# Optimization experiments

Measured on AMD Instinct MI355X. Metric: run time of the kernel, lower is better.

## Reference

```python
import jax, jax.numpy as jnp
import numpy as np

B, S, D, H = 8, 1024, 1024, 16
DH = D // H  # 64

def setup_inputs() -> dict:
    key = jax.random.key(0)
    k1, k2, k3 = jax.random.split(key, 3)
    x = jax.random.normal(k1, (B, S, D), dtype=jnp.float32)
    mask = jnp.tril(jnp.ones((S, S), dtype=bool))[None, None]  # causal [1,1,S,S]
    W_qkv = jax.random.normal(k2, (D, 3 * D), dtype=jnp.float32) * 0.02
    W_out = jax.random.normal(k3, (D, D), dtype=jnp.float32) * 0.02
    return {"x": x, "mask": mask, "W_qkv": W_qkv, "W_out": W_out}

def reference(x, mask, W_qkv, W_out):
    qkv = jnp.einsum('bnd,de->bne', x, W_qkv)
    q, k, v = jnp.split(qkv, 3, axis=-1)
    # [b, h, n, dh]
    split_heads = lambda t: t.reshape(B, S, H, DH).transpose(0, 2, 1, 3)
    q, k, v = map(split_heads, (q, k, v))
    attn = jnp.einsum('bhnd,bhmd->bhnm', q, k) / jnp.sqrt(jnp.float32(DH))
    attn = jnp.where(mask, attn, 0.7 * jnp.finfo(attn.dtype).min)
    attn = jax.nn.softmax(attn.astype(jnp.float32), axis=-1).astype(x.dtype)
    out = jnp.einsum('bhnm,bhmd->bhnd', attn, v)
    out = out.transpose(0, 2, 1, 3).reshape(B, S, D)
    return jnp.einsum('bnd,de->bne', out, W_out)
```

## Files before the change

kernel.cpp:

```cpp
#include <hip/hip_runtime.h>
#include <stdint.h>

typedef __attribute__((ext_vector_type(8))) short short8;
typedef __attribute__((ext_vector_type(4))) float floatx4;

__device__ __forceinline__ unsigned short f2bf(float f) {
  union { float f; uint32_t u; } v; v.f = f;
  uint32_t u = v.u;
  return (unsigned short)((u + 0x7FFFu + ((u >> 16) & 1u)) >> 16);
}

__device__ __forceinline__ uint32_t fbits(float f) {
  union { float f; uint32_t u; } v; v.f = f; return v.u;
}
__device__ __forceinline__ uint32_t pkbf(float hi, float lo) {
  return __builtin_amdgcn_perm(fbits(hi), fbits(lo), 0x07060302u);
}

__device__ __forceinline__ void gl_lds16(const void* g, void* l) {
  __builtin_amdgcn_global_load_lds((__attribute__((address_space(1))) void*)g,
                                   (__attribute__((address_space(3))) void*)l,
                                   16, 0, 0);
}

__global__ __launch_bounds__(256) void prep_kernel(const float* __restrict__ x,
                                                   unsigned short* __restrict__ xb,
                                                   const float* __restrict__ Wqkv,
                                                   unsigned short* __restrict__ WqkvT,
                                                   const float* __restrict__ Wout,
                                                   unsigned short* __restrict__ WoutT) {
  __shared__ float tile[32][33];
  int id = blockIdx.x;
  if (id < 8192) {
    int i = id * 256 + threadIdx.x;
    float4 v = ((const float4*)x)[i];
    ushort4 o;
    o.x = f2bf(v.x); o.y = f2bf(v.y); o.z = f2bf(v.z); o.w = f2bf(v.w);
    ((ushort4*)xb)[i] = o;
    return;
  }
  id -= 8192;
  int bx = id & 127, r0 = (id >> 7) * 32;
  const int R = 1024;
  const float* in; unsigned short* out; int C;
  if (bx < 96) { in = Wqkv; out = WqkvT; C = 3072; }
  else         { in = Wout; out = WoutT; C = 1024; bx -= 96; }
  int c0 = bx * 32;
  int tx = threadIdx.x & 31;
  int ty = threadIdx.x >> 5;
  for (int i = ty; i < 32; i += 8)
    tile[i][tx] = in[(size_t)(r0 + i) * C + c0 + tx];
  __syncthreads();
  for (int i = ty; i < 32; i += 8)
    out[(size_t)(c0 + i) * R + r0 + tx] = f2bf(tile[tx][i]);
}

__global__ __launch_bounds__(256) void gemm_bt_kernel(const unsigned short* __restrict__ A,
                                                      const unsigned short* __restrict__ Bt,
                                                      int N, int mode,
                                                      unsigned short* __restrict__ qo,
                                                      unsigned short* __restrict__ ko,
                                                      unsigned short* __restrict__ vo,
                                                      float* __restrict__ fo) {
  const int Kd = 1024;
  __shared__ union {
    struct { unsigned short A[2][8192]; unsigned short B[2][8192]; } s;
    float cf[16384];
    unsigned short ch[32768];
  } sm;
  const int tid = threadIdx.x;
  const int w = tid >> 6, lane = tid & 63;
  const int quad = lane >> 4, l16 = lane & 15;
  const int l7 = l16 & 7;
  const int wm = w >> 1, wn = w & 1;
  const int m0 = blockIdx.y * 128, n0 = blockIdx.x * 128;
  const int tr = (mode == 0) && (n0 >= 2048);
  const int r8 = lane >> 3, ch = lane & 7;
  const int sw = (ch ^ r8) * 8;

  floatx4 acc[4][4];
#pragma unroll
  for (int i = 0; i < 4; ++i)
#pragma unroll
    for (int j = 0; j < 4; ++j)
      acc[i][j] = (floatx4){0.f, 0.f, 0.f, 0.f};

  auto stage = [&](int it, int buf) {
    const int k0 = it * 64;
#pragma unroll
    for (int i = 0; i < 4; ++i) {
      const int row = i * 32 + w * 8 + r8;
      gl_lds16(A + (size_t)(m0 + row) * Kd + k0 + sw, (char*)&sm.s.A[buf][0] + i * 4096 + w * 1024);
      gl_lds16(Bt + (size_t)(n0 + row) * Kd + k0 + sw, (char*)&sm.s.B[buf][0] + i * 4096 + w * 1024);
    }
  };

  stage(0, 0);
  __syncthreads();

  for (int it = 0; it < 16; ++it) {
    const int buf = it & 1;
    if (it < 15) stage(it + 1, buf ^ 1);
    const char* Ab = (const char*)&sm.s.A[buf][0];
    const char* Bb = (const char*)&sm.s.B[buf][0];
#pragma unroll
    for (int half = 0; half < 2; ++half) {
      short8 af[4], bf[4];
#pragma unroll
      for (int i = 0; i < 4; ++i)
        af[i] = *(const short8*)(Ab + (wm * 64 + i * 16 + l16) * 128 +
                                 (((half << 2) | quad) ^ l7) * 16);
#pragma unroll
      for (int j = 0; j < 4; ++j)
        bf[j] = *(const short8*)(Bb + (wn * 64 + j * 16 + l16) * 128 +
                                 (((half << 2) | quad) ^ l7) * 16);
      if (!tr) {
#pragma unroll
        for (int i = 0; i < 4; ++i)
#pragma unroll
          for (int j = 0; j < 4; ++j)
            acc[i][j] = __builtin_amdgcn_mfma_f32_16x16x32_bf16(af[i], bf[j], acc[i][j], 0, 0, 0);
      } else {
#pragma unroll
        for (int p = 0; p < 4; ++p)
#pragma unroll
          for (int q = 0; q < 4; ++q)
            acc[p][q] = __builtin_amdgcn_mfma_f32_16x16x32_bf16(bf[p], af[q], acc[p][q], 0, 0, 0);
      }
    }
    __syncthreads();
  }

  if (mode == 1) {
    float* Cs = sm.cf;
#pragma unroll
    for (int i = 0; i < 4; ++i)
#pragma unroll
      for (int j = 0; j < 4; ++j)
#pragma unroll
        for (int r = 0; r < 4; ++r) {
          int row = wm * 64 + i * 16 + quad * 4 + r;
          int col = wn * 64 + j * 16 + l16;
          Cs[row * 128 + (col ^ ((row & 7) << 2))] = acc[i][j][r];
        }
    __syncthreads();
#pragma unroll
    for (int c = 0; c < 16; ++c) {
      int idx = c * 256 + tid;
      int row = idx >> 5, fc = idx & 31;
      float4 v = *(const float4*)&sm.cf[row * 128 + ((fc ^ (row & 7)) << 2)];
      *(float4*)&fo[(size_t)(m0 + row) * N + n0 + fc * 4] = v;
    }
  } else {
    unsigned short* Cs = sm.ch;
    if (!tr) {
#pragma unroll
      for (int i = 0; i < 4; ++i)
#pragma unroll
        for (int j = 0; j < 4; ++j)
#pragma unroll
          for (int r = 0; r < 4; ++r) {
            int row = wm * 64 + i * 16 + quad * 4 + r;
            int col = wn * 64 + j * 16 + l16;
            Cs[row * 128 + (col ^ ((row & 7) << 3))] = f2bf(acc[i][j][r]);
          }
    } else {
#pragma unroll
      for (int p = 0; p < 4; ++p)
#pragma unroll
        for (int q = 0; q < 4; ++q)
#pragma unroll
          for (int r = 0; r < 4; ++r) {
            int row = wn * 64 + p * 16 + quad * 4 + r;
            int col = wm * 64 + q * 16 + l16;
            Cs[row * 128 + (col ^ ((row & 7) << 3))] = f2bf(acc[p][q][r]);
          }
    }
    __syncthreads();
    unsigned short* dst0 = (n0 < 1024) ? qo : ko;
#pragma unroll
    for (int c = 0; c < 8; ++c) {
      int idx = c * 256 + tid;
      int row = idx >> 4, lc = idx & 15;
      short8 v = *(const short8*)&sm.ch[row * 128 + ((lc ^ (row & 7)) << 3)];
      int col = lc * 8;
      if (!tr) {
        int m = m0 + row, n = n0 + col;
        int h = (n & 1023) >> 6, dh = n & 63;
        int bb = m >> 10, s = m & 1023;
        *(short8*)&dst0[(size_t)(bb * 16 + h) * 65536 + (size_t)s * 64 + dh] = v;
      } else {
        int n = n0 + row, m = m0 + col;
        int h = (n & 1023) >> 6, dh = n & 63;
        int bb = m >> 10, s0 = m & 1023;
        *(short8*)&vo[(size_t)(bb * 16 + h) * 65536 + (size_t)dh * 1024 + s0] = v;
      }
    }
  }
}

__global__ __launch_bounds__(512, 2) void gemm_qkv_kernel(const unsigned short* __restrict__ A,
                                                          const unsigned short* __restrict__ Bt,
                                                          unsigned short* __restrict__ qo,
                                                          unsigned short* __restrict__ ko,
                                                          unsigned short* __restrict__ vo) {
  __shared__ union {
    struct { unsigned short A[2][16384]; unsigned short B[2][8192]; } s;
    unsigned short ch[49152];
  } sm;
  const int tid = threadIdx.x;
  const int w = tid >> 6, lane = tid & 63;
  const int quad = lane >> 4, l16 = lane & 15, l7 = l16 & 7;
  const int wm = w >> 1, wn = w & 1;
  const int m0 = blockIdx.y * 256, n0 = blockIdx.x * 128;
  const bool tr = (n0 >= 2048);
  const int r8 = lane >> 3, ch8 = lane & 7;
  const int sw = (ch8 ^ r8) * 8;

  floatx4 acc[16];
#pragma unroll
  for (int i = 0; i < 16; ++i) acc[i] = (floatx4){0.f, 0.f, 0.f, 0.f};

  auto stageA = [&](int t, int buf) {
    const int k0 = t * 64;
#pragma unroll
    for (int i = 0; i < 4; ++i) {
      const int row = i * 64 + w * 8 + r8;
      gl_lds16(A + (size_t)(m0 + row) * 1024 + k0 + sw,
               (char*)&sm.s.A[buf][0] + (i * 64 + w * 8) * 128);
    }
  };
  auto stageB = [&](int t, int buf) {
    const int k0 = t * 64;
#pragma unroll
    for (int i = 0; i < 2; ++i) {
      const int row = i * 64 + w * 8 + r8;
      gl_lds16(Bt + (size_t)(n0 + row) * 1024 + k0 + sw,
               (char*)&sm.s.B[buf][0] + (i * 64 + w * 8) * 128);
    }
  };

  const int cK0 = (quad ^ l7) * 16;
  const int cK1 = ((4 | quad) ^ l7) * 16;
  const int arow = (wm * 64 + l16) * 128;
  const int brow = (wn * 64 + l16) * 128;

  short8 af[4][2], bfr[4][2];

  auto readF = [&](int buf2, int kk) {
    const char* Ab2 = (const char*)&sm.s.A[buf2][0];
    const char* Bb2 = (const char*)&sm.s.B[buf2][0];
    const int cK = kk ? cK1 : cK0;
#pragma unroll
    for (int mf = 0; mf < 4; ++mf)
      af[mf][kk] = *(const short8*)(Ab2 + arow + mf * 2048 + cK);
#pragma unroll
    for (int nf = 0; nf < 4; ++nf)
      bfr[nf][kk] = *(const short8*)(Bb2 + brow + nf * 2048 + cK);
  };

#define CLUSTER(KK)                                                                 \
  do {                                                                              \
    if (!tr) {                                                                      \
      _Pragma("unroll") for (int mf = 0; mf < 4; ++mf)                              \
      _Pragma("unroll") for (int nf = 0; nf < 4; ++nf)                              \
        acc[mf * 4 + nf] = __builtin_amdgcn_mfma_f32_16x16x32_bf16(                 \
            af[mf][KK], bfr[nf][KK], acc[mf * 4 + nf], 0, 0, 0);                    \
    } else {                                                                        \
      _Pragma("unroll") for (int nf = 0; nf < 4; ++nf)                              \
      _Pragma("unroll") for (int mf = 0; mf < 4; ++mf)                              \
        acc[nf * 4 + mf] = __builtin_amdgcn_mfma_f32_16x16x32_bf16(                 \
            bfr[nf][KK], af[mf][KK], acc[nf * 4 + mf], 0, 0, 0);                    \
    }                                                                               \
  } while (0)

  stageA(0, 0); stageB(0, 0);
  stageA(1, 1); stageB(1, 1);
  asm volatile("s_waitcnt vmcnt(6)" ::: "memory");
  __builtin_amdgcn_s_barrier();
  readF(0, 0);
  __builtin_amdgcn_sched_barrier(0);
  readF(0, 1);
  __builtin_amdgcn_sched_barrier(0);

  for (int t = 0; t < 16; ++t) {
    const int buf = t & 1;
    asm volatile("s_waitcnt lgkmcnt(8)" ::: "memory");
    __builtin_amdgcn_sched_barrier(0);
    __builtin_amdgcn_s_setprio(1);
    CLUSTER(0);
    __builtin_amdgcn_s_setprio(0);
    __builtin_amdgcn_sched_barrier(0);
    asm volatile("s_waitcnt lgkmcnt(0)" ::: "memory");
    __builtin_amdgcn_sched_barrier(0);
    __builtin_amdgcn_s_barrier();
    if (t < 14) {
      stageA(t + 2, buf); stageB(t + 2, buf);
      asm volatile("s_waitcnt vmcnt(6)" ::: "memory");
    } else {
      asm volatile("s_waitcnt vmcnt(0)" ::: "memory");
    }
    __builtin_amdgcn_s_barrier();
    if (t < 15) {
      readF(buf ^ 1, 0);
      __builtin_amdgcn_sched_barrier(0);
    }
    __builtin_amdgcn_s_setprio(1);
    CLUSTER(1);
    __builtin_amdgcn_s_setprio(0);
    __builtin_amdgcn_sched_barrier(0);
    if (t < 15) {
      readF(buf ^ 1, 1);
      __builtin_amdgcn_sched_barrier(0);
    }
  }
#undef CLUSTER

  unsigned short* Cs = sm.ch;
  if (!tr) {
#pragma unroll
    for (int mf = 0; mf < 4; ++mf)
#pragma unroll
      for (int nf = 0; nf < 4; ++nf)
#pragma unroll
        for (int r = 0; r < 4; ++r) {
          int row = wm * 64 + mf * 16 + quad * 4 + r;
          int col = wn * 64 + nf * 16 + l16;
          Cs[row * 128 + (col ^ ((row & 7) << 3))] = f2bf(acc[mf * 4 + nf][r]);
        }
    __syncthreads();
    unsigned short* dst0 = (n0 < 1024) ? qo : ko;
#pragma unroll
    for (int c = 0; c < 8; ++c) {
      int idx = c * 512 + tid;
      int row = idx >> 4, lc = idx & 15;
      short8 v = *(const short8*)&Cs[row * 128 + ((lc ^ (row & 7)) << 3)];
      int m = m0 + row, n = n0 + lc * 8;
      int h = (n & 1023) >> 6, dh = n & 63;
      int bb = m >> 10, s = m & 1023;
      *(short8*)&dst0[(size_t)(bb * 16 + h) * 65536 + (size_t)s * 64 + dh] = v;
    }
  } else {
#pragma unroll
    for (int nf = 0; nf < 4; ++nf)
#pragma unroll
      for (int mf = 0; mf < 4; ++mf)
#pragma unroll
        for (int r = 0; r < 4; ++r) {
          int row = wn * 64 + nf * 16 + quad * 4 + r;
          int col = wm * 64 + mf * 16 + l16;
          Cs[row * 256 + (col ^ ((row & 7) << 3))] = f2bf(acc[nf * 4 + mf][r]);
        }
    __syncthreads();
#pragma unroll
    for (int c = 0; c < 8; ++c) {
      int idx = c * 512 + tid;
      int row = idx >> 5, lc = idx & 31;
      short8 v = *(const short8*)&Cs[row * 256 + ((lc ^ (row & 7)) << 3)];
      int n = n0 + row, m = m0 + lc * 8;
      int h = (n & 1023) >> 6, dh = n & 63;
      int bb = m >> 10, s = m & 1023;
      *(short8*)&vo[(size_t)(bb * 16 + h) * 65536 + (size_t)dh * 1024 + s] = v;
    }
  }
}

__global__ __launch_bounds__(256, 2) void attn_kernel(const unsigned short* __restrict__ Qb,
                                                      const unsigned short* __restrict__ Kb,
                                                      const unsigned short* __restrict__ VbT,
                                                      unsigned short* __restrict__ AOb) {
  __shared__ unsigned short Kt[2][4096];
  __shared__ unsigned short Vt[2][4096];
  const int tid = threadIdx.x;
  const int w = tid >> 6, lane = tid & 63;
  const int quad = lane >> 4, l16 = lane & 15;
  const int l7 = l16 & 7;
  const int id = blockIdx.x;
  const int by = id >> 2;
  const int p = id & 3;
  const int bb = by >> 4, hh = by & 15;
  const int qlo = p * 128 + w * 32;
  const int qhi = (7 - p) * 128 + w * 32;
  const unsigned short* Qp = Qb + (size_t)by * 65536;
  const unsigned short* Kp = Kb + (size_t)by * 65536;
  const unsigned short* Vp = VbT + (size_t)by * 65536;

  short8 bq[2][2][2];
#pragma unroll
  for (int g = 0; g < 2; ++g)
#pragma unroll
    for (int qt = 0; qt < 2; ++qt)
#pragma unroll
      for (int kh = 0; kh < 2; ++kh)
        bq[g][qt][kh] = *(const short8*)(Qp + (size_t)((g ? qhi : qlo) + qt * 16 + l16) * 64 +
                                         kh * 32 + quad * 8);

  floatx4 o[2][2][4];
  floatx4 ps[2][2];
#pragma unroll
  for (int g = 0; g < 2; ++g)
#pragma unroll
    for (int qt = 0; qt < 2; ++qt) {
      ps[g][qt] = (floatx4){0.f, 0.f, 0.f, 0.f};
#pragma unroll
      for (int dt = 0; dt < 4; ++dt) o[g][qt][dt] = (floatx4){0.f, 0.f, 0.f, 0.f};
    }

  short8 ones;
#pragma unroll
  for (int i = 0; i < 8; ++i) ones[i] = (short)0x3F80;

  const int T = 16 - 2 * p;
  const int r8 = lane >> 3, ch = lane & 7;
  const int sw8 = (ch ^ r8) * 8;

  auto stage = [&](int t, int buf) {
    const int n0 = t * 64;
#pragma unroll
    for (int i = 0; i < 2; ++i) {
      const int c = w * 2 + i;
      const int row = c * 8 + r8;
      gl_lds16(Kp + (size_t)(n0 + row) * 64 + sw8, (char*)&Kt[buf][0] + c * 1024);
      gl_lds16(Vp + (size_t)row * 1024 + n0 + sw8, (char*)&Vt[buf][0] + c * 1024);
    }
  };

  stage(0, 0);
  __syncthreads();

  for (int t = 0; t < T; ++t) {
    const int buf = t & 1;
    if (t + 1 < T) stage(t + 1, buf ^ 1);
    const int n0 = t * 64;
    const bool alo = (n0 <= qlo + 31), ahi = (n0 <= qhi + 31);
    if (alo | ahi) {
      const char* kbase = (const char*)&Kt[buf][0];
      const char* vbase = (const char*)&Vt[buf][0];
      short8 ak[4][2];
#pragma unroll
      for (int kt = 0; kt < 4; ++kt)
#pragma unroll
        for (int kh = 0; kh < 2; ++kh)
          ak[kt][kh] = *(const short8*)(kbase + (kt * 16 + l16) * 128 +
                                        (((kh << 2) | quad) ^ l7) * 16);
      union PaU { short8 v; uint32_t d[4]; };
      PaU pa[2][2][2];

      auto score = [&](int g, int qb) {
        const bool full = (n0 + 63 <= qb);
#pragma unroll
        for (int kt = 0; kt < 4; ++kt)
#pragma unroll
          for (int qt = 0; qt < 2; ++qt) {
            floatx4 s = (floatx4){0.f, 0.f, 0.f, 0.f};
            s = __builtin_amdgcn_mfma_f32_16x16x32_bf16(ak[kt][0], bq[g][qt][0], s, 0, 0, 0);
            s = __builtin_amdgcn_mfma_f32_16x16x32_bf16(ak[kt][1], bq[g][qt][1], s, 0, 0, 0);
            float f[4];
            if (full) {
#pragma unroll
              for (int r = 0; r < 4; ++r)
                f[r] = exp2f(fmaf(s[r], 0.18033688f, -11.5415603f));
            } else {
              const int query = qb + qt * 16 + l16;
#pragma unroll
              for (int r = 0; r < 4; ++r) {
                const int key = n0 + kt * 16 + quad * 4 + r;
                float e = exp2f(fmaf(s[r], 0.18033688f, -11.5415603f));
                f[r] = (key <= query) ? e : 0.0f;
              }
            }
            pa[g][qt][kt >> 1].d[(kt & 1) * 2 + 0] = pkbf(f[1], f[0]);
            pa[g][qt][kt >> 1].d[(kt & 1) * 2 + 1] = pkbf(f[3], f[2]);
          }
#pragma unroll
        for (int qt = 0; qt < 2; ++qt)
#pragma unroll
          for (int u = 0; u < 2; ++u)
            ps[g][qt] = __builtin_amdgcn_mfma_f32_16x16x32_bf16(pa[g][qt][u].v, ones, ps[g][qt], 0, 0, 0);
      };
      if (alo) score(0, qlo);
      if (ahi) score(1, qhi);

#pragma unroll
      for (int dt = 0; dt < 4; ++dt) {
        const int row128 = (dt * 16 + l16) * 128;
#pragma unroll
        for (int u = 0; u < 2; ++u) {
          union { short8 v8; ushort4 h[2]; } bv;
          bv.h[0] = *(const ushort4*)(vbase + row128 +
                                      (((u << 2) | (quad >> 1)) ^ l7) * 16 + (quad & 1) * 8);
          bv.h[1] = *(const ushort4*)(vbase + row128 +
                                      (((u << 2) | 2 | (quad >> 1)) ^ l7) * 16 + (quad & 1) * 8);
          if (alo) {
#pragma unroll
            for (int qt = 0; qt < 2; ++qt)
              o[0][qt][dt] = __builtin_amdgcn_mfma_f32_16x16x32_bf16(pa[0][qt][u].v, bv.v8, o[0][qt][dt], 0, 0, 0);
          }
          if (ahi) {
#pragma unroll
            for (int qt = 0; qt < 2; ++qt)
              o[1][qt][dt] = __builtin_amdgcn_mfma_f32_16x16x32_bf16(pa[1][qt][u].v, bv.v8, o[1][qt][dt], 0, 0, 0);
          }
        }
      }
    }
    __syncthreads();
  }

#pragma unroll
  for (int g = 0; g < 2; ++g) {
    const int qb = g ? qhi : qlo;
#pragma unroll
    for (int qt = 0; qt < 2; ++qt) {
      float inv[4];
#pragma unroll
      for (int r = 0; r < 4; ++r) inv[r] = 1.0f / ps[g][qt][r];
#pragma unroll
      for (int dt = 0; dt < 4; ++dt)
#pragma unroll
        for (int r = 0; r < 4; ++r) {
          int row = qb + qt * 16 + quad * 4 + r;
          AOb[(size_t)(bb * 1024 + row) * 1024 + hh * 64 + dt * 16 + l16] =
              f2bf(o[g][qt][dt][r] * inv[r]);
        }
    }
  }
}

extern "C" void kernel_launch(void* const* d_in, const int* in_sizes, int n_in,
                              void* d_out, int out_size, void* d_ws, size_t ws_size,
                              hipStream_t stream) {
  const float* x    = (const float*)d_in[0];
  const float* Wqkv = (const float*)d_in[2];
  const float* Wout = (const float*)d_in[3];
  float* out = (float*)d_out;

  unsigned short* xb    = (unsigned short*)d_ws;
  unsigned short* WqkvT = xb    + (size_t)8 * 1024 * 1024;
  unsigned short* WoutT = WqkvT + (size_t)3 * 1024 * 1024;
  unsigned short* Qb    = WoutT + (size_t)1024 * 1024;
  unsigned short* Kb    = Qb    + (size_t)8 * 1024 * 1024;
  unsigned short* VbT   = Kb    + (size_t)8 * 1024 * 1024;
  unsigned short* AOb   = VbT   + (size_t)8 * 1024 * 1024;

  prep_kernel<<<12288, 256, 0, stream>>>(x, xb, Wqkv, WqkvT, Wout, WoutT);
  gemm_qkv_kernel<<<dim3(24, 32), 512, 0, stream>>>(xb, WqkvT, Qb, Kb, VbT);
  attn_kernel<<<512, 256, 0, stream>>>(Qb, Kb, VbT, AOb);
  gemm_bt_kernel<<<dim3(8, 64), 256, 0, stream>>>(AOb, WoutT, 1024, 1, nullptr, nullptr, nullptr, out);
}
```

Baseline: 229.2 us.

## Enlarge QKV GEMM tile to 256x256 with swizzled block order and split B prefetch

```diff
diff --git a/kernel.cpp b/kernel.cpp
--- a/kernel.cpp
+++ b/kernel.cpp
@@ -205,136 +205,153 @@
                                                           unsigned short* __restrict__ ko,
                                                           unsigned short* __restrict__ vo) {
   __shared__ union {
-    struct { unsigned short A[2][16384]; unsigned short B[2][8192]; } s;
-    unsigned short ch[49152];
+    struct { unsigned short A[2][16384]; unsigned short B[2][16384]; } s;
+    unsigned short ch[65536];
   } sm;
   const int tid = threadIdx.x;
   const int w = tid >> 6, lane = tid & 63;
   const int quad = lane >> 4, l16 = lane & 15, l7 = l16 & 7;
-  const int wm = w >> 1, wn = w & 1;
-  const int m0 = blockIdx.y * 256, n0 = blockIdx.x * 128;
+  const int wm = w >> 2, wn = w & 3;
+  const int bid = blockIdx.x;
+  const int sbid = (bid & 7) * 48 + (bid >> 3);
+  const int m0 = (sbid / 12) * 256, n0 = (sbid % 12) * 256;
   const bool tr = (n0 >= 2048);
   const int r8 = lane >> 3, ch8 = lane & 7;
-  const int sw = (ch8 ^ r8) * 8;
-
-  floatx4 acc[16];
-#pragma unroll
-  for (int i = 0; i < 16; ++i) acc[i] = (floatx4){0.f, 0.f, 0.f, 0.f};
+  const int swk = (ch8 ^ r8) * 8;
+
+  floatx4 acc[32];
+#pragma unroll
+  for (int i = 0; i < 32; ++i) acc[i] = (floatx4){0.f, 0.f, 0.f, 0.f};
 
   auto stageA = [&](int t, int buf) {
     const int k0 = t * 64;
 #pragma unroll
     for (int i = 0; i < 4; ++i) {
       const int row = i * 64 + w * 8 + r8;
-      gl_lds16(A + (size_t)(m0 + row) * 1024 + k0 + sw,
+      gl_lds16(A + (size_t)(m0 + row) * 1024 + k0 + swk,
                (char*)&sm.s.A[buf][0] + (i * 64 + w * 8) * 128);
     }
   };
   auto stageB = [&](int t, int buf) {
     const int k0 = t * 64;
 #pragma unroll
-    for (int i = 0; i < 2; ++i) {
+    for (int i = 0; i < 4; ++i) {
       const int row = i * 64 + w * 8 + r8;
-      gl_lds16(Bt + (size_t)(n0 + row) * 1024 + k0 + sw,
+      gl_lds16(Bt + (size_t)(n0 + row) * 1024 + k0 + swk,
                (char*)&sm.s.B[buf][0] + (i * 64 + w * 8) * 128);
     }
   };
 
   const int cK0 = (quad ^ l7) * 16;
   const int cK1 = ((4 | quad) ^ l7) * 16;
-  const int arow = (wm * 64 + l16) * 128;
+  const int arow = (wm * 128 + l16) * 128;
   const int brow = (wn * 64 + l16) * 128;
 
-  short8 af[4][2], bfr[4][2];
-
-  auto readF = [&](int buf2, int kk) {
-    const char* Ab2 = (const char*)&sm.s.A[buf2][0];
-    const char* Bb2 = (const char*)&sm.s.B[buf2][0];
-    const int cK = kk ? cK1 : cK0;
-#pragma unroll
-    for (int mf = 0; mf < 4; ++mf)
-      af[mf][kk] = *(const short8*)(Ab2 + arow + mf * 2048 + cK);
-#pragma unroll
-    for (int nf = 0; nf < 4; ++nf)
-      bfr[nf][kk] = *(const short8*)(Bb2 + brow + nf * 2048 + cK);
-  };
-
-#define CLUSTER(KK)                                                                 \
+  short8 af[8];
+  short8 bfr[2];
+
+#define CLUSTER(NH)                                                                 \
   do {                                                                              \
     if (!tr) {                                                                      \
-      _Pragma("unroll") for (int mf = 0; mf < 4; ++mf)                              \
-      _Pragma("unroll") for (int nf = 0; nf < 4; ++nf)                              \
-        acc[mf * 4 + nf] = __builtin_amdgcn_mfma_f32_16x16x32_bf16(                 \
-            af[mf][KK], bfr[nf][KK], acc[mf * 4 + nf], 0, 0, 0);                    \
+      _Pragma("unroll") for (int mf = 0; mf < 8; ++mf)                              \
+      _Pragma("unroll") for (int j = 0; j < 2; ++j)                                 \
+        acc[mf * 4 + (NH)*2 + j] = __builtin_amdgcn_mfma_f32_16x16x32_bf16(         \
+            af[mf], bfr[j], acc[mf * 4 + (NH)*2 + j], 0, 0, 0);                     \
     } else {                                                                        \
-      _Pragma("unroll") for (int nf = 0; nf < 4; ++nf)                              \
-      _Pragma("unroll") for (int mf = 0; mf < 4; ++mf)                              \
-        acc[nf * 4 + mf] = __builtin_amdgcn_mfma_f32_16x16x32_bf16(                 \
-            bfr[nf][KK], af[mf][KK], acc[nf * 4 + mf], 0, 0, 0);                    \
+      _Pragma("unroll") for (int j = 0; j < 2; ++j)                                 \
+      _Pragma("unroll") for (int mf = 0; mf < 8; ++mf)                              \
+        acc[((NH)*2 + j) * 8 + mf] = __builtin_amdgcn_mfma_f32_16x16x32_bf16(       \
+            bfr[j], af[mf], acc[((NH)*2 + j) * 8 + mf], 0, 0, 0);                   \
     }                                                                               \
   } while (0)
 
-  stageA(0, 0); stageB(0, 0);
-  stageA(1, 1); stageB(1, 1);
-  asm volatile("s_waitcnt vmcnt(6)" ::: "memory");
+  stageA(0, 0); stageB(0, 0); stageA(1, 1);
+  asm volatile("s_waitcnt vmcnt(4)" ::: "memory");
   __builtin_amdgcn_s_barrier();
-  readF(0, 0);
-  __builtin_amdgcn_sched_barrier(0);
-  readF(0, 1);
-  __builtin_amdgcn_sched_barrier(0);
 
   for (int t = 0; t < 16; ++t) {
     const int buf = t & 1;
-    asm volatile("s_waitcnt lgkmcnt(8)" ::: "memory");
+    const char* Ab = (const char*)&sm.s.A[buf][0];
+    const char* Bb = (const char*)&sm.s.B[buf][0];
+
+#pragma unroll
+    for (int mf = 0; mf < 8; ++mf)
+      af[mf] = *(const short8*)(Ab + arow + mf * 2048 + cK0);
+    bfr[0] = *(const short8*)(Bb + brow + 0 * 2048 + cK0);
+    bfr[1] = *(const short8*)(Bb + brow + 1 * 2048 + cK0);
+    if (t <= 14) stageB(t + 1, buf ^ 1);
+    __builtin_amdgcn_s_barrier();
+    asm volatile("s_waitcnt lgkmcnt(0)" ::: "memory");
     __builtin_amdgcn_sched_barrier(0);
     __builtin_amdgcn_s_setprio(1);
     CLUSTER(0);
     __builtin_amdgcn_s_setprio(0);
     __builtin_amdgcn_sched_barrier(0);
+    __builtin_amdgcn_s_barrier();
+
+    bfr[0] = *(const short8*)(Bb + brow + 2 * 2048 + cK0);
+    bfr[1] = *(const short8*)(Bb + brow + 3 * 2048 + cK0);
+    __builtin_amdgcn_s_barrier();
     asm volatile("s_waitcnt lgkmcnt(0)" ::: "memory");
     __builtin_amdgcn_sched_barrier(0);
-    __builtin_amdgcn_s_barrier();
-    if (t < 14) {
-      stageA(t + 2, buf); stageB(t + 2, buf);
-      asm volatile("s_waitcnt vmcnt(6)" ::: "memory");
-    } else {
-      asm volatile("s_waitcnt vmcnt(0)" ::: "memory");
-    }
-    __builtin_amdgcn_s_barrier();
-    if (t < 15) {
-      readF(buf ^ 1, 0);
-      __builtin_amdgcn_sched_barrier(0);
-    }
     __builtin_amdgcn_s_setprio(1);
     CLUSTER(1);
     __builtin_amdgcn_s_setprio(0);
     __builtin_amdgcn_sched_barrier(0);
-    if (t < 15) {
-      readF(buf ^ 1, 1);
-      __builtin_amdgcn_sched_barrier(0);
-    }
+    __builtin_amdgcn_s_barrier();
+
+#pragma unroll
+    for (int mf = 0; mf < 8; ++mf)
+      af[mf] = *(const short8*)(Ab + arow + mf * 2048 + cK1);
+    bfr[0] = *(const short8*)(Bb + brow + 0 * 2048 + cK1);
+    bfr[1] = *(const short8*)(Bb + brow + 1 * 2048 + cK1);
+    __builtin_amdgcn_s_barrier();
+    asm volatile("s_waitcnt lgkmcnt(0)" ::: "memory");
+    __builtin_amdgcn_sched_barrier(0);
+    __builtin_amdgcn_s_setprio(1);
+    CLUSTER(0);
+    __builtin_amdgcn_s_setprio(0);
+    __builtin_amdgcn_sched_barrier(0);
+    __builtin_amdgcn_s_barrier();
+
+    bfr[0] = *(const short8*)(Bb + brow + 2 * 2048 + cK1);
+    bfr[1] = *(const short8*)(Bb + brow + 3 * 2048 + cK1);
+    if (t <= 13) {
+      stageA(t + 2, buf);
+      asm volatile("s_waitcnt vmcnt(4)" ::: "memory");
+    } else {
+      asm volatile("s_waitcnt vmcnt(0)" ::: "memory");
+    }
+    __builtin_amdgcn_s_barrier();
+    asm volatile("s_waitcnt lgkmcnt(0)" ::: "memory");
+    __builtin_amdgcn_sched_barrier(0);
+    __builtin_amdgcn_s_setprio(1);
+    CLUSTER(1);
+    __builtin_amdgcn_s_setprio(0);
+    __builtin_amdgcn_sched_barrier(0);
+    __builtin_amdgcn_s_barrier();
   }
 #undef CLUSTER
 
   unsigned short* Cs = sm.ch;
   if (!tr) {
 #pragma unroll
-    for (int mf = 0; mf < 4; ++mf)
+    for (int mf = 0; mf < 8; ++mf)
 #pragma unroll
       for (int nf = 0; nf < 4; ++nf)
 #pragma unroll
         for (int r = 0; r < 4; ++r) {
-          int row = wm * 64 + mf * 16 + quad * 4 + r;
+          int row = wm * 128 + mf * 16 + quad * 4 + r;
           int col = wn * 64 + nf * 16 + l16;
-          Cs[row * 128 + (col ^ ((row & 7) << 3))] = f2bf(acc[mf * 4 + nf][r]);
+          Cs[row * 256 + (col ^ ((row & 7) << 3))] = f2bf(acc[mf * 4 + nf][r]);
         }
     __syncthreads();
     unsigned short* dst0 = (n0 < 1024) ? qo : ko;
 #pragma unroll
-    for (int c = 0; c < 8; ++c) {
+    for (int c = 0; c < 16; ++c) {
       int idx = c * 512 + tid;
-      int row = idx >> 4, lc = idx & 15;
-      short8 v = *(const short8*)&Cs[row * 128 + ((lc ^ (row & 7)) << 3)];
+      int row = idx >> 5, lc = idx & 31;
+      short8 v = *(const short8*)&Cs[row * 256 + ((lc ^ (row & 7)) << 3)];
       int m = m0 + row, n = n0 + lc * 8;
       int h = (n & 1023) >> 6, dh = n & 63;
       int bb = m >> 10, s = m & 1023;
@@ -344,16 +361,16 @@
 #pragma unroll
     for (int nf = 0; nf < 4; ++nf)
 #pragma unroll
-      for (int mf = 0; mf < 4; ++mf)
+      for (int mf = 0; mf < 8; ++mf)
 #pragma unroll
         for (int r = 0; r < 4; ++r) {
           int row = wn * 64 + nf * 16 + quad * 4 + r;
-          int col = wm * 64 + mf * 16 + l16;
-          Cs[row * 256 + (col ^ ((row & 7) << 3))] = f2bf(acc[nf * 4 + mf][r]);
+          int col = wm * 128 + mf * 16 + l16;
+          Cs[row * 256 + (col ^ ((row & 7) << 3))] = f2bf(acc[nf * 8 + mf][r]);
         }
     __syncthreads();
 #pragma unroll
-    for (int c = 0; c < 8; ++c) {
+    for (int c = 0; c < 16; ++c) {
       int idx = c * 512 + tid;
       int row = idx >> 5, lc = idx & 31;
       short8 v = *(const short8*)&Cs[row * 256 + ((lc ^ (row & 7)) << 3)];
@@ -544,7 +561,7 @@
   unsigned short* AOb   = VbT   + (size_t)8 * 1024 * 1024;
 
   prep_kernel<<<12288, 256, 0, stream>>>(x, xb, Wqkv, WqkvT, Wout, WoutT);
-  gemm_qkv_kernel<<<dim3(24, 32), 512, 0, stream>>>(xb, WqkvT, Qb, Kb, VbT);
+  gemm_qkv_kernel<<<384, 512, 0, stream>>>(xb, WqkvT, Qb, Kb, VbT);
   attn_kernel<<<512, 256, 0, stream>>>(Qb, Kb, VbT, AOb);
   gemm_bt_kernel<<<dim3(8, 64), 256, 0, stream>>>(AOb, WoutT, 1024, 1, nullptr, nullptr, nullptr, out);
 }
```

Measured after the change: 259.9 us. 1.13x slower.
